# Performance work log

Measured on AMD Instinct MI355X. Metric: run time of the kernel, lower is better.

## Reference

```python
import jax, jax.numpy as jnp
import numpy as np

N, E, Z, C, B, G, T = 10000, 160000, 10, 64, 8, 16, 2
R_MAX = 5.0
AVG_NEIGH = 16.0
L_SLICES = ((0, 1), (1, 4), (4, 9))  # l=0,1,2 blocks of the 9 SH components


def sph_harm(u):
    # component-normalized real spherical harmonics up to l=2, u: [E,3] unit vectors
    x, y, z = u[:, 0], u[:, 1], u[:, 2]
    s3, s5, s15 = 3.0 ** 0.5, 5.0 ** 0.5, 15.0 ** 0.5
    return jnp.stack([
        jnp.ones_like(x),
        s3 * x, s3 * y, s3 * z,
        s15 * x * y, s15 * y * z, (s5 / 2) * (3 * z * z - 1), s15 * x * z, (s15 / 2) * (x * x - y * y),
    ], axis=1)  # [E,9]


def radial_embed(r):
    # Bessel basis * polynomial cutoff (p=5), r: [E]
    u = r / R_MAX
    n = jnp.arange(1, B + 1, dtype=jnp.float32)
    bessel = jnp.sqrt(2.0 / R_MAX) * jnp.sin(n[None, :] * jnp.pi * u[:, None]) / (r[:, None] + 1e-9)
    p = 5.0
    fc = 1 - (p + 1) * (p + 2) / 2 * u ** p + p * (p + 2) * u ** (p + 1) - p * (p + 1) / 2 * u ** (p + 2)
    fc = jnp.where(u < 1.0, fc, 0.0)
    return bessel * fc[:, None]  # [E,B]


def per_l_linear(x, W):
    # x: [n,C,9], W: [3,C,C]; independent channel mixing per l-block
    return jnp.concatenate([
        jnp.einsum('ncm,cd->ndm', x[:, :, s:e], W[l]) for l, (s, e) in enumerate(L_SLICES)
    ], axis=2)


def _forward(positions, node_attrs, charges, shifts, W_emb, atomic_energies,
             W_r1, W_r2, W_mix, W_sc, w_poly, W_prod, w_e, w_d,
             edge_index, batch, num_graphs):
    sender, receiver = edge_index[0], edge_index[1]
    # atomic reference energies
    node_e0 = node_attrs @ atomic_energies  # [N]
    e0 = jax.ops.segment_sum(node_e0, batch, num_segments=num_graphs)
    # node embedding: scalars only
    node_feats = jnp.zeros((positions.shape[0], C, 9), positions.dtype)
    node_feats = node_feats.at[:, :, 0].set(node_attrs @ W_emb)
    # edge geometry
    vec = positions[sender] - positions[receiver] + shifts  # [E,3]
    lengths = jnp.sqrt(jnp.sum(vec * vec, axis=1) + 1e-12)
    sh = sph_harm(vec / lengths[:, None])        # [E,9]
    edge_feats = radial_embed(lengths)           # [E,B]
    energies = [e0]
    dipoles = []
    for t in range(T):
        # radial MLP -> per-channel TP weights
        w = jax.nn.silu(edge_feats @ W_r1[t]) @ W_r2[t]      # [E,C]
        h_s = node_feats[sender, :, 0]                       # gather sender scalars [E,C]
        m = (w * h_s)[:, :, None] * sh[:, None, :]           # TP message [E,C,9]
        agg = jax.ops.segment_sum(m, receiver, num_segments=positions.shape[0]) / AVG_NEIGH
        msg = per_l_linear(agg, W_mix[t])
        sc = per_l_linear(node_feats, W_sc[t])               # self-connection
        # product basis (correlation 3): channel-wise scalar polynomial gate
        s0 = msg[:, :, 0]
        poly = w_poly[t, :, 0][None] + w_poly[t, :, 1][None] * s0 + w_poly[t, :, 2][None] * s0 * s0
        node_feats = per_l_linear(msg * poly[:, :, None], W_prod[t]) + sc
        # readout: 1x0e energy + 1x1o dipole
        e_n = node_feats[:, :, 0] @ w_e[t]                   # [N]
        energies.append(jax.ops.segment_sum(e_n, batch, num_segments=num_graphs))
        dipoles.append(jnp.einsum('ncm,c->nm', node_feats[:, :, 1:4], w_d[t]))  # [N,3]
    contributions = jnp.stack(energies, axis=-1)             # [G,T+1]
    total_energy = jnp.sum(contributions, axis=-1)           # [G]
    atomic_dipoles = jnp.sum(jnp.stack(dipoles, axis=-1), axis=-1)  # [N,3]
    total_dipole = jax.ops.segment_sum(atomic_dipoles, batch, num_segments=num_graphs)
    total_dipole = total_dipole + jax.ops.segment_sum(charges[:, None] * positions, batch, num_segments=num_graphs)
    return total_energy, contributions, atomic_dipoles, total_dipole


def setup_inputs():
    key = jax.random.key(0)
    ks = jax.random.split(key, 16)
    s = 0.1
    species = jax.random.randint(ks[1], (N,), 0, Z)
    return {
        'positions': jax.random.normal(ks[0], (N, 3)) * 3.0,
        'node_attrs': jax.nn.one_hot(species, Z, dtype=jnp.float32),
        'charges': jax.random.normal(ks[2], (N,)) * 0.1,
        'shifts': jnp.zeros((E, 3), jnp.float32),
        'W_emb': jax.random.normal(ks[5], (Z, C)) * s,
        'atomic_energies': jax.random.normal(ks[6], (Z,)) * s,
        'W_r1': jax.random.normal(ks[7], (T, B, 64)) * s,
        'W_r2': jax.random.normal(ks[8], (T, 64, C)) * s,
        'W_mix': jax.random.normal(ks[9], (T, 3, C, C)) * s,
        'W_sc': jax.random.normal(ks[10], (T, 3, C, C)) * s,
        'w_poly': jax.random.normal(ks[11], (T, C, 3)) * s,
        'W_prod': jax.random.normal(ks[12], (T, 3, C, C)) * s,
        'w_e': jax.random.normal(ks[13], (T, C)) * s,
        'w_d': jax.random.normal(ks[14], (T, C)) * s,
        'edge_index': jax.random.randint(ks[3], (2, E), 0, N),
        'batch': jnp.sort(jax.random.randint(ks[4], (N,), 0, G)),
        'num_graphs': G,
    }


def reference(positions, node_attrs, charges, shifts, W_emb, atomic_energies,
              W_r1, W_r2, W_mix, W_sc, w_poly, W_prod, w_e, w_d,
              edge_index, batch, num_graphs):
    args = (node_attrs, charges, shifts, W_emb, atomic_energies, W_r1, W_r2,
            W_mix, W_sc, w_poly, W_prod, w_e, w_d, edge_index, batch, num_graphs)
    total_energy, contributions, atomic_dipoles, total_dipole = _forward(positions, *args)
    forces = -jax.grad(lambda p: jnp.sum(_forward(p, *args)[0]))(positions)
    return total_energy, contributions, forces, total_dipole, atomic_dipoles
```

## Files before the change

kernel.cpp:

```cpp
#include <hip/hip_runtime.h>
#include <hip/hip_bf16.h>

#define NN 10000
#define NE 160000
#define NZ 10
#define NBES 8
#define NG 16
#define NT 2
#define NB 2048
#define NB1 2049
#define PL ((size_t)NN*64)

static constexpr float PI_F  = 3.14159265358979323846f;
static constexpr float KBES  = 0.63245553203367587f;
static constexpr float S3    = 1.73205080756887729f;

static constexpr size_t OFF_UVL  = 0;
static constexpr size_t OFF_PIN  = OFF_UVL + (size_t)NE*4;
static constexpr size_t OFF_ATT  = OFF_PIN + (size_t)NN*3;
static constexpr size_t OFF_CHG  = OFF_ATT + (size_t)NN*NZ;
static constexpr size_t OFF_SHF  = OFF_CHG + (size_t)NN;
static constexpr size_t OFF_NF0  = OFF_SHF + (size_t)NE*3;
static constexpr size_t OFF_NF1  = OFF_NF0 + PL;
static constexpr size_t OFF_MSG0 = OFF_NF1 + 4*PL;
static constexpr size_t OFF_MSG1 = OFF_MSG0 + 4*PL;
static constexpr size_t OFF_AGG  = OFF_MSG1 + 4*PL;
static constexpr size_t O_GA1    = OFF_MSG0 + PL;
static constexpr size_t O_GA0    = OFF_AGG;
static constexpr size_t OFF_W    = OFF_AGG + 4*PL;
static constexpr size_t O_WEMB   = OFF_W;
static constexpr size_t O_AE     = O_WEMB + 640;
static constexpr size_t O_R1     = O_AE   + 16;
static constexpr size_t O_R2     = O_R1   + 1024;
static constexpr size_t O_WMIX   = O_R2   + 8192;
static constexpr size_t O_WMIXT  = O_WMIX + 24576;
static constexpr size_t O_WSC    = O_WMIXT+ 24576;
static constexpr size_t O_WSCT   = O_WSC  + 24576;
static constexpr size_t O_WPROD  = O_WSCT + 24576;
static constexpr size_t O_WPRODT = O_WPROD+ 24576;
static constexpr size_t O_WPOLY  = O_WPRODT+24576;
static constexpr size_t O_WE     = O_WPOLY+ 384;
static constexpr size_t O_WD     = O_WE   + 128;
static constexpr size_t OFF_ACC  = O_WD   + 128;
static constexpr size_t O_E0G    = OFF_ACC;
static constexpr size_t O_ETG    = O_E0G + 16;
static constexpr size_t O_TD     = O_ETG + 32;
static constexpr size_t O_ADP    = O_TD  + 48;
static constexpr size_t O_GPOS   = O_ADP + (size_t)NN*3;
static constexpr size_t ACC_FLOATS = 96 + (size_t)NN*6;
static constexpr size_t O_EN0    = O_GPOS + (size_t)NN*3;
static constexpr size_t O_EN1    = O_EN0 + NN;
static constexpr size_t O_E0N    = O_EN1 + NN;
static constexpr size_t O_FLAG   = O_E0N + NN;
static constexpr size_t O_TW     = O_FLAG + 4;
static constexpr size_t O_TQ     = O_TW + (size_t)2*NB1*64;
static constexpr size_t O_OFFR   = O_TQ + (size_t)2*NB1*64;
static constexpr size_t O_OFFS   = O_OFFR + (NN+1);
static constexpr size_t O_CURR   = O_OFFS + (NN+1);
static constexpr size_t O_CURS   = O_CURR + NN;
static constexpr size_t O_RECRAW = O_CURS + NN;
static constexpr size_t O_RECR   = (O_RECRAW + 7) & ~(size_t)7;
static constexpr size_t O_RECS   = O_RECR + (size_t)NE*8 + 64;
static constexpr size_t WS_FLOATS= O_RECS + (size_t)NE*8 + 64;

__device__ __forceinline__ float rlane(float v, int l){
  return __int_as_float(__builtin_amdgcn_readlane(__float_as_int(v), l));
}
__device__ __forceinline__ int irlane(float v, int l){
  return __builtin_amdgcn_readlane(__float_as_int(v), l);
}

static constexpr int LD_CNT[14] = {NN*3, NN*NZ, NN, NE*3, NZ*64, NZ, NT*NBES*64, NT*64*64,
                                   NT*3*64*64, NT*3*64*64, NT*64*3, NT*3*64*64, NT*64, NT*64};
static constexpr int LD_TOTAL = NN*3 + NN*NZ + NN + NE*3 + NZ*64 + NZ + NT*NBES*64 + NT*64*64
                              + 3*(NT*3*64*64) + NT*64*3 + 4*(NT*64) - NT*64*2;
static constexpr int LD_B  = (LD_TOTAL + 255)/256;
static constexpr int Z1_B  = ((int)ACC_FLOATS + 255)/256;
static constexpr int Z2_B  = (2*NN + 255)/256;
__global__ __launch_bounds__(256) void k_load_all(
    const void* s0, const void* s1, const void* s2, const void* s3, const void* s4,
    const void* s5, const void* s6, const void* s7, const void* s8, const void* s9,
    const void* s10, const void* s11, const void* s12, const void* s13,
    float* __restrict__ ws){
  if (blockIdx.x >= LD_B){
    int zb = blockIdx.x - LD_B;
    if (zb < Z1_B){
      int i = zb*256 + threadIdx.x;
      if (i < (int)ACC_FLOATS) ws[OFF_ACC + i] = 0.f;
    } else {
      int i = (zb - Z1_B)*256 + threadIdx.x;
      if (i < 2*NN) ((int*)(ws + O_CURR))[i] = 0;
    }
    return;
  }
  __shared__ int found;
  if (threadIdx.x == 0) found = 0;
  __syncthreads();
  const unsigned* raw = (const unsigned*)s1;
  int f = 0;
  for (int i = threadIdx.x; i < 4096; i += 256){
    unsigned w = raw[i];
    f |= (w == 0x00003F80u || w == 0x3F803F80u) ? 1 : 0;
  }
  if (f) found = 1;
  __syncthreads();
  const int isbf = found;
  if (blockIdx.x == 0 && threadIdx.x == 0) ((int*)(ws + O_FLAG))[0] = isbf;

  const void* srcs[14] = {s0,s1,s2,s3,s4,s5,s6,s7,s8,s9,s10,s11,s12,s13};
  const size_t dsts[14] = {OFF_PIN, OFF_ATT, OFF_CHG, OFF_SHF, O_WEMB, O_AE, O_R1, O_R2,
                           O_WMIX, O_WSC, O_WPOLY, O_WPROD, O_WE, O_WD};
  int i = blockIdx.x*256 + threadIdx.x;
  int seg = -1, off = i;
  #pragma unroll
  for (int j = 0; j < 14; ++j){
    if (seg < 0){
      if (off < LD_CNT[j]) seg = j;
      else off -= LD_CNT[j];
    }
  }
  if (seg < 0) return;
  float v = isbf ? __bfloat162float(((const __hip_bfloat16*)srcs[seg])[off])
                 : ((const float*)srcs[seg])[off];
  ws[dsts[seg] + off] = v;
}

static constexpr int GEOM_B = (NE+255)/256;
static constexpr int TAB_B  = (2*NB1+3)/4;
static constexpr int INIT_B = (NN+3)/4;
static constexpr int TRAN_B = 5*4096/256;
__global__ __launch_bounds__(256, 3) void k_prep(float* __restrict__ ws, const int* __restrict__ ei){
  int b = blockIdx.x;
  if (b < GEOM_B){
    int e = b*256 + threadIdx.x;
    if (e >= NE) return;
    const float* pos = ws + OFF_PIN;
    const float* shifts = ws + OFF_SHF;
    int s = ei[e], r = ei[NE + e];
    float vx = pos[s*3+0] - pos[r*3+0] + shifts[(size_t)e*3+0];
    float vy = pos[s*3+1] - pos[r*3+1] + shifts[(size_t)e*3+1];
    float vz = pos[s*3+2] - pos[r*3+2] + shifts[(size_t)e*3+2];
    float L = sqrtf(vx*vx + vy*vy + vz*vz + 1e-12f);
    float inv = 1.f / L;
    float4 uq; uq.x = vx*inv; uq.y = vy*inv; uq.z = vz*inv; uq.w = L;
    *(float4*)(ws + OFF_UVL + (size_t)e*4) = uq;
    if (L < 5.f){
      atomicAdd((int*)(ws + O_CURR) + r, 1);
      atomicAdd((int*)(ws + O_CURS) + s, 1);
    }
  } else if (b < GEOM_B + TAB_B){
    int lane = threadIdx.x & 63;
    int task = (b - GEOM_B)*4 + (threadIdx.x >> 6);
    if (task >= 2*NB1) return;
    int t = task / NB1, node = task % NB1;
    const float* R1 = ws + O_R1 + (size_t)t*512;
    const float* R2 = ws + O_R2 + (size_t)t*4096;
    float r1c[8];
    #pragma unroll
    for (int j = 0; j < 8; ++j) r1c[j] = R1[j*64 + lane];
    float L = fmaxf((float)node * (5.f/NB), 1e-6f);
    float ur = L*0.2f;
    float ef[8], dd[8];
    if (ur < 1.f){
      float u2=ur*ur, u4=u2*u2, u5=u4*ur;
      float fc = 1.f - 21.f*u5 + 35.f*u5*ur - 15.f*u5*u2;
      float omu = 1.f - ur;
      float dfc = -105.f*u4*omu*omu;
      float invr = 1.f/(L + 1e-9f);
      #pragma unroll
      for (int bb = 0; bb < 8; ++bb){
        float nb = (float)(bb+1);
        float arg = nb*PI_F*ur;
        float sn = __sinf(arg), cs = __cosf(arg);
        float bes = KBES*sn*invr;
        float dbes = KBES*(nb*PI_F*0.2f)*cs*invr - bes*invr;
        ef[bb] = bes*fc;
        dd[bb] = dbes*fc + bes*dfc*0.2f;
      }
    } else {
      #pragma unroll
      for (int bb = 0; bb < 8; ++bb){ ef[bb] = 0.f; dd[bb] = 0.f; }
    }
    float a = 0.f, tt = 0.f;
    #pragma unroll
    for (int bb = 0; bb < 8; ++bb){ a = fmaf(ef[bb], r1c[bb], a); tt = fmaf(r1c[bb], dd[bb], tt); }
    float sg = 1.f/(1.f + __expf(-a));
    float sl = a*sg;
    float q  = sg*fmaf(a, 1.f - sg, 1.f)*tt;
    float r2c[64];
    #pragma unroll
    for (int j = 0; j < 64; ++j) r2c[j] = R2[j*64 + lane];
    float W0=0.f, W1=0.f, Q0=0.f, Q1=0.f;
    #pragma unroll
    for (int j = 0; j < 64; j += 2){
      W0 = fmaf(rlane(sl, j  ), r2c[j  ], W0);
      W1 = fmaf(rlane(sl, j+1), r2c[j+1], W1);
      Q0 = fmaf(rlane(q,  j  ), r2c[j  ], Q0);
      Q1 = fmaf(rlane(q,  j+1), r2c[j+1], Q1);
    }
    size_t idx = ((size_t)t*NB1 + node)*64 + lane;
    ws[O_TW + idx] = (W0+W1)*(1.f/16.f);
    ws[O_TQ + idx] = (Q0+Q1)*(1.f/16.f);
  } else if (b < GEOM_B + TAB_B + INIT_B){
    int lane = threadIdx.x & 63;
    int n = (b - GEOM_B - TAB_B)*4 + (threadIdx.x >> 6);
    if (n >= NN) return;
    const float* attrs = ws + OFF_ATT;
    float acc = 0.f;
    #pragma unroll
    for (int z = 0; z < NZ; ++z) acc = fmaf(attrs[(size_t)n*NZ+z], ws[O_WEMB + z*64 + lane], acc);
    ws[OFF_NF0 + (size_t)n*64 + lane] = acc;
    if (lane == 0){
      float e = 0.f;
      #pragma unroll
      for (int z = 0; z < NZ; ++z) e = fmaf(attrs[(size_t)n*NZ+z], ws[O_AE + z], e);
      ws[O_E0N + n] = e;
    }
  } else {
    int i = (b - GEOM_B - TAB_B - INIT_B)*256 + threadIdx.x;
    int mat = i >> 12, r = (i >> 6) & 63, c = i & 63;
    const size_t src[5] = {O_WMIX, O_WMIX+12288, O_WPROD, O_WPROD+12288, O_WSC+12288};
    const size_t dst[5] = {O_WMIXT, O_WMIXT+12288, O_WPRODT, O_WPRODT+12288, O_WSCT+12288};
    ws[dst[mat] + (size_t)c*64 + r] = ws[src[mat] + (size_t)r*64 + c];
  }
}

__global__ __launch_bounds__(1024) void k_csr_scan(
    int* __restrict__ curr, int* __restrict__ curs,
    int* __restrict__ offr, int* __restrict__ offs_){
  __shared__ unsigned short cr[NN], cs[NN];
  __shared__ int pr[1024], ps[1024];
  int tid = threadIdx.x;
  for (int i = tid; i < NN; i += 1024){
    cr[i] = (unsigned short)curr[i];
    cs[i] = (unsigned short)curs[i];
  }
  __syncthreads();
  const int chunk = (NN + 1023)/1024;
  int lo = tid*chunk, hi = lo + chunk;
  if (hi > NN) hi = NN;
  if (lo > NN) lo = NN;
  int sr = 0, ss = 0;
  for (int i = lo; i < hi; ++i){ sr += cr[i]; ss += cs[i]; }
  pr[tid] = sr; ps[tid] = ss;
  __syncthreads();
  for (int o = 1; o < 1024; o <<= 1){
    int vr = (tid >= o) ? pr[tid-o] : 0;
    int vs = (tid >= o) ? ps[tid-o] : 0;
    __syncthreads();
    pr[tid] += vr; ps[tid] += vs;
    __syncthreads();
  }
  int runr = tid ? pr[tid-1] : 0;
  int runs = tid ? ps[tid-1] : 0;
  for (int i = lo; i < hi; ++i){
    int a = cr[i], c = cs[i];
    offr[i] = runr; curr[i] = runr; runr += a;
    offs_[i] = runs; curs[i] = runs; runs += c;
  }
  if (tid == 1023){ offr[NN] = runr; offs_[NN] = runs; }
}

__global__ void k_csr_fill(const int* __restrict__ ei, const float* __restrict__ uvl,
                           int* __restrict__ curr, int* __restrict__ curs,
                           float* __restrict__ recr, float* __restrict__ recs){
  int e = blockIdx.x*256 + threadIdx.x;
  if (e >= NE) return;
  float4 q = *(const float4*)(uvl + (size_t)e*4);
  if (q.w >= 5.f) return;
  int s = ei[e], r = ei[NE + e];
  int4 meta; meta.x = s; meta.y = r; meta.z = e; meta.w = 0;
  int pr = atomicAdd(&curr[r], 1);
  *(float4*)(recr + (size_t)pr*8) = q;
  *(int4*)(recr + (size_t)pr*8 + 4) = meta;
  int ps = atomicAdd(&curs[s], 1);
  *(float4*)(recs + (size_t)ps*8) = q;
  *(int4*)(recs + (size_t)ps*8 + 4) = meta;
}

__global__ __launch_bounds__(256) void k_agg(
    const float* __restrict__ TWt, const float* __restrict__ recr,
    const float* __restrict__ h, const int* __restrict__ offr,
    float* __restrict__ agg){
  int lane = threadIdx.x & 63;
  int wid = blockIdx.x*4 + (threadIdx.x >> 6);
  int nw  = gridDim.x*4;
  for (int n = wid; n < NN; n += nw){
    int lo = offr[n], hi = offr[n+1];
    float c0=0.f, x1=0.f, y1=0.f, z1=0.f;
    for (int i = lo; i < hi; i += 8){
      float rv = recr[(size_t)i*8 + lane];
      int cnt = hi - i;
      if (cnt >= 8){
        #pragma unroll
        for (int j = 0; j < 8; ++j){
          float ux = rlane(rv, j*8+0), uy = rlane(rv, j*8+1), uz = rlane(rv, j*8+2);
          float L  = rlane(rv, j*8+3);
          int   s  = irlane(rv, j*8+4);
          float pos = L*(NB/5.f); int bi = (int)pos; float f = pos - (float)bi;
          const float* T = TWt + (size_t)bi*64 + lane;
          float t0 = T[0];
          float w = fmaf(T[64]-t0, f, t0);
          float wh = w * h[(size_t)s*64 + lane];
          c0 += wh;
          x1 = fmaf(wh, ux, x1);
          y1 = fmaf(wh, uy, y1);
          z1 = fmaf(wh, uz, z1);
        }
      } else {
        for (int j = 0; j < cnt; ++j){
          float ux = rlane(rv, j*8+0), uy = rlane(rv, j*8+1), uz = rlane(rv, j*8+2);
          float L  = rlane(rv, j*8+3);
          int   s  = irlane(rv, j*8+4);
          float pos = L*(NB/5.f); int bi = (int)pos; float f = pos - (float)bi;
          const float* T = TWt + (size_t)bi*64 + lane;
          float t0 = T[0];
          float w = fmaf(T[64]-t0, f, t0);
          float wh = w * h[(size_t)s*64 + lane];
          c0 += wh;
          x1 = fmaf(wh, ux, x1);
          y1 = fmaf(wh, uy, y1);
          z1 = fmaf(wh, uz, z1);
        }
      }
    }
    size_t ob = (size_t)n*64 + lane;
    agg[ob]        = c0;
    agg[ob+PL]     = S3*x1;
    agg[ob+2*PL]   = S3*y1;
    agg[ob+3*PL]   = S3*z1;
  }
}

template<int GB1>
__global__ __launch_bounds__(256, 3) void k_lin2(
    const float* __restrict__ in, const float* __restrict__ W3, float* __restrict__ out,
    const float* __restrict__ WMIXT1, const float* __restrict__ WPRODT1,
    const float* __restrict__ we1, const float* __restrict__ wp1,
    float* __restrict__ ga1){
  int k = blockIdx.y;
  int l = (k==0) ? 0 : 1;
  const float* W = W3 + (size_t)l*4096;
  int lane = threadIdx.x & 63;
  float wcol[64];
  #pragma unroll
  for (int j = 0; j < 64; ++j) wcol[j] = W[j*64 + lane];
  float wcol2[64];
  float g = 0.f, p0 = 0.f, p1 = 0.f, p2 = 0.f;
  const bool gb1 = GB1 && (k == 0);
  if (gb1){
    #pragma unroll
    for (int j = 0; j < 64; ++j) wcol2[j] = WMIXT1[j*64 + lane];
    #pragma unroll
    for (int c = 0; c < 64; ++c) g = fmaf(we1[c], WPRODT1[c*64 + lane], g);
    p0 = wp1[lane*3]; p1 = wp1[lane*3+1]; p2 = wp1[lane*3+2];
  }
  int wid = blockIdx.x*4 + (threadIdx.x >> 6);
  int nw  = gridDim.x*4;
  const float* inp = in + (size_t)k*PL;
  float* outp = out + (size_t)k*PL;
  for (int n = wid; n < NN; n += nw){
    float x = inp[(size_t)n*64 + lane];
    float a0 = 0.f, a1 = 0.f, a2 = 0.f, a3 = 0.f;
    #pragma unroll
    for (int j = 0; j < 64; j += 4){
      a0 = fmaf(rlane(x, j  ), wcol[j  ], a0);
      a1 = fmaf(rlane(x, j+1), wcol[j+1], a1);
      a2 = fmaf(rlane(x, j+2), wcol[j+2], a2);
      a3 = fmaf(rlane(x, j+3), wcol[j+3], a3);
    }
    float m = (a0+a1) + (a2+a3);
    outp[(size_t)n*64 + lane] = m;
    if (gb1){
      float poly = fmaf(fmaf(p2, m, p1), m, p0);
      float dp   = fmaf(2.f*p2, m, p1);
      float gb = g*fmaf(m, dp, poly);
      float b0=0.f, b1=0.f, b2=0.f, b3=0.f;
      #pragma unroll
      for (int j = 0; j < 64; j += 4){
        b0 = fmaf(rlane(gb, j  ), wcol2[j  ], b0);
        b1 = fmaf(rlane(gb, j+1), wcol2[j+1], b1);
        b2 = fmaf(rlane(gb, j+2), wcol2[j+2], b2);
        b3 = fmaf(rlane(gb, j+3), wcol2[j+3], b3);
      }
      ga1[(size_t)n*64 + lane] = (b0+b1) + (b2+b3);
    }
  }
}

template<int WRITE_NF, int NF_SINGLE>
__global__ __launch_bounds__(256, 3) void k_tail(
    const float* __restrict__ nf_in, const float* __restrict__ msg,
    const float* __restrict__ Wsc, const float* __restrict__ Wprod, const float* __restrict__ wp,
    const float* __restrict__ we, const float* __restrict__ wd,
    float* __restrict__ nf_out, float* __restrict__ en, float* __restrict__ adp){
  int lane = threadIdx.x & 63;
  int k = threadIdx.x >> 6;
  int l = (k==0) ? 0 : 1;
  const bool use_sc = !(NF_SINGLE && k > 0);
  float wcs[64], wcp[64];
  #pragma unroll
  for (int j = 0; j < 64; ++j)
    wcp[j] = Wprod[(size_t)l*4096 + j*64 + lane];
  if (use_sc){
    #pragma unroll
    for (int j = 0; j < 64; ++j)
      wcs[j] = Wsc[(size_t)l*4096 + j*64 + lane];
  }
  float p0 = wp[lane*3], p1 = wp[lane*3+1], p2 = wp[lane*3+2];
  float rw = (k==0) ? we[lane] : wd[lane];
  const float* msgk = msg + (size_t)k*PL;
  const float* nfk  = nf_in + (size_t)k*PL;
  float* outk = nf_out + (size_t)k*PL;
  for (int n = blockIdx.x; n < NN; n += gridDim.x){
    size_t base = (size_t)n*64 + lane;
    float s0 = msg[base];
    float xm = (k==0) ? s0 : msgk[base];
    float xg = xm * fmaf(fmaf(p2, s0, p1), s0, p0);
    float b0=0.f, b1=0.f;
    #pragma unroll
    for (int j = 0; j < 64; j += 2){
      b0 = fmaf(rlane(xg, j  ), wcp[j  ], b0);
      b1 = fmaf(rlane(xg, j+1), wcp[j+1], b1);
    }
    float out = b0 + b1;
    if (use_sc){
      float xs = nfk[base];
      float a0=0.f, a1=0.f;
      #pragma unroll
      for (int j = 0; j < 64; j += 2){
        a0 = fmaf(rlane(xs, j  ), wcs[j  ], a0);
        a1 = fmaf(rlane(xs, j+1), wcs[j+1], a1);
      }
      out += a0 + a1;
    }
    if (WRITE_NF) outk[base] = out;
    float red = out * rw;
    #pragma unroll
    for (int o = 32; o; o >>= 1) red += __shfl_xor(red, o, 64);
    if (lane == 0){
      if (k == 0) en[n] = red;
      else        adp[n*3 + (k-1)] += red;
    }
  }
}

static constexpr int GHG_GRID = 1024;
static constexpr int RED_B = (NN+255)/256;
__global__ __launch_bounds__(256) void k_ghg0(float* __restrict__ ws, const int* __restrict__ offs_,
                                              const int* __restrict__ batch){
  __shared__ float wl[2*4096];
  if (blockIdx.x >= GHG_GRID){
    int n = (blockIdx.x - GHG_GRID)*256 + threadIdx.x;
    int lane = threadIdx.x & 63;
    bool valid = (n < NN);
    int g = valid ? batch[n] : -1;
    float v0=0.f, v1=0.f, v2=0.f, tx=0.f, ty=0.f, tz=0.f;
    if (valid){
      v0 = ws[O_E0N + n]; v1 = ws[O_EN0 + n]; v2 = ws[O_EN1 + n];
      float qq = ws[OFF_CHG + n];
      tx = ws[O_ADP + n*3+0] + qq*ws[OFF_PIN + n*3+0];
      ty = ws[O_ADP + n*3+1] + qq*ws[OFF_PIN + n*3+1];
      tz = ws[O_ADP + n*3+2] + qq*ws[OFF_PIN + n*3+2];
    }
    float* e0g = ws + O_E0G; float* Etg = ws + O_ETG; float* td = ws + O_TD;
    int g0 = __shfl(g, 0, 64), g63 = __shfl(g, 63, 64);
    if (g0 == g63 && g0 >= 0){
      #pragma unroll
      for (int o = 32; o; o >>= 1){
        v0 += __shfl_xor(v0, o, 64); v1 += __shfl_xor(v1, o, 64); v2 += __shfl_xor(v2, o, 64);
        tx += __shfl_xor(tx, o, 64); ty += __shfl_xor(ty, o, 64); tz += __shfl_xor(tz, o, 64);
      }
      if (lane == 0){
        atomicAdd(&e0g[g0], v0); atomicAdd(&Etg[g0], v1); atomicAdd(&Etg[16+g0], v2);
        atomicAdd(&td[g0*3+0], tx); atomicAdd(&td[g0*3+1], ty); atomicAdd(&td[g0*3+2], tz);
      }
    } else if (valid){
      atomicAdd(&e0g[g], v0); atomicAdd(&Etg[g], v1); atomicAdd(&Etg[16+g], v2);
      atomicAdd(&td[g*3+0], tx); atomicAdd(&td[g*3+1], ty); atomicAdd(&td[g*3+2], tz);
    }
    return;
  }
  for (int i = threadIdx.x; i < 4096; i += 256){
    wl[i]        = ws[O_WPRODT + i];
    wl[4096 + i] = ws[O_WMIXT + i];
  }
  __syncthreads();
  const int lane = threadIdx.x & 63;
  int wid = blockIdx.x*4 + (threadIdx.x >> 6);
  const int nw = GHG_GRID*4;
  float gnfc = ws[O_WE + lane];
  {
    const float* WS1 = ws + O_WSCT + 12288;
    const float* we1 = ws + O_WE + 64;
    #pragma unroll
    for (int c = 0; c < 64; ++c) gnfc = fmaf(we1[c], WS1[c*64 + lane], gnfc);
  }
  const float p0 = ws[O_WPOLY + lane*3];
  const float p1 = ws[O_WPOLY + lane*3 + 1];
  const float p2 = ws[O_WPOLY + lane*3 + 2];
  const float* TW1 = ws + O_TW + (size_t)NB1*64;
  const float* recs = ws + O_RECS;
  const float* GA1 = ws + O_GA1;
  for (int n = wid; n < NN; n += nw){
    int lo = offs_[n], hi = offs_[n+1];
    float acc = 0.f;
    for (int i = lo; i < hi; i += 8){
      float rv = recs[(size_t)i*8 + lane];
      int cnt = hi - i;
      if (cnt >= 8){
        #pragma unroll
        for (int j = 0; j < 8; ++j){
          float L = rlane(rv, j*8+3);
          int   r = irlane(rv, j*8+5);
          float pos = L*(NB/5.f); int bi = (int)pos; float f = pos - (float)bi;
          const float* T = TW1 + (size_t)bi*64 + lane;
          float t0 = T[0];
          float w = fmaf(T[64]-t0, f, t0);
          acc = fmaf(w, GA1[(size_t)r*64 + lane], acc);
        }
      } else {
        for (int j = 0; j < cnt; ++j){
          float L = rlane(rv, j*8+3);
          int   r = irlane(rv, j*8+5);
          float pos = L*(NB/5.f); int bi = (int)pos; float f = pos - (float)bi;
          const float* T = TW1 + (size_t)bi*64 + lane;
          float t0 = T[0];
          float w = fmaf(T[64]-t0, f, t0);
          acc = fmaf(w, GA1[(size_t)r*64 + lane], acc);
        }
      }
    }
    float gB = gnfc + acc;
    float q0=0.f, q1=0.f;
    #pragma unroll
    for (int j = 0; j < 64; j += 2){
      q0 = fmaf(rlane(gB,j),   wl[j*64 + lane],     q0);
      q1 = fmaf(rlane(gB,j+1), wl[(j+1)*64 + lane], q1);
    }
    float gmp = q0 + q1;
    float s0v = ws[OFF_MSG0 + (size_t)n*64 + lane];
    float poly = fmaf(fmaf(p2, s0v, p1), s0v, p0);
    float dp   = fmaf(2.f*p2, s0v, p1);
    float gb = gmp * fmaf(s0v, dp, poly);
    float u0=0.f, u1=0.f;
    #pragma unroll
    for (int j = 0; j < 64; j += 2){
      u0 = fmaf(rlane(gb,j),   wl[4096 + j*64 + lane],     u0);
      u1 = fmaf(rlane(gb,j+1), wl[4096 + (j+1)*64 + lane], u1);
    }
    ws[O_GA0 + (size_t)n*64 + lane] = u0 + u1;
  }
}

__global__ __launch_bounds__(256) void k_bwdE2(float* __restrict__ ws, const int* __restrict__ nlive_ptr){
  const int lane = threadIdx.x & 63;
  int wid = blockIdx.x*4 + (threadIdx.x >> 6);
  const int nw = gridDim.x*4;
  const int nlive = nlive_ptr[0];
  const int ngrp = (nlive + 7) >> 3;
  const float* recs = ws + O_RECS;
  const float* TQ  = ws + O_TQ;
  const float* h0  = ws + OFF_NF0;
  const float* h1  = ws + OFF_NF1;
  const float* ga0 = ws + O_GA0;
  const float* ga1 = ws + O_GA1;
  float* gpos = ws + O_GPOS;
  for (int gi = wid; gi < ngrp; gi += nw){
    const int i0 = gi*8;
    float rv = recs[(size_t)i0*8 + lane];
    int cnt = nlive - i0; if (cnt > 8) cnt = 8;
    #pragma unroll 8
    for (int j = 0; j < cnt; ++j){
      float ux = rlane(rv, j*8+0), uy = rlane(rv, j*8+1), uz = rlane(rv, j*8+2);
      float L  = rlane(rv, j*8+3);
      int   s  = irlane(rv, j*8+4);
      int   r  = irlane(rv, j*8+5);
      float pos = L*(NB/5.f); int bi = (int)pos; float f = pos - (float)bi;
      const float* T0 = TQ + (size_t)bi*64 + lane;
      const float* T1 = T0 + (size_t)NB1*64;
      float Q0 = fmaf(T0[64]-T0[0], f, T0[0]);
      float Q1 = fmaf(T1[64]-T1[0], f, T1[0]);
      float rr = Q0*h0[(size_t)s*64 + lane]*ga0[(size_t)r*64 + lane]
               + Q1*h1[(size_t)s*64 + lane]*ga1[(size_t)r*64 + lane];
      #pragma unroll
      for (int o = 32; o; o >>= 1) rr += __shfl_xor(rr, o, 64);
      if (lane < 3){
        float u = (lane==0) ? ux : ((lane==1) ? uy : uz);
        float v = rr*u;
        atomicAdd(&gpos[(size_t)s*3 + lane],  v);
        atomicAdd(&gpos[(size_t)r*3 + lane], -v);
      }
    }
  }
}

__global__ void k_writeout(const float* __restrict__ e0g, const float* __restrict__ Etg,
                           const float* __restrict__ td, const float* __restrict__ adp,
                           const float* __restrict__ gpos, void* __restrict__ outv,
                           const int* __restrict__ flag){
  int i = blockIdx.x*256 + threadIdx.x;
  const int total = NG + NG*3 + NN*3 + NG*3 + NN*3;
  if (i >= total) return;
  float v;
  if (i < 16){
    v = e0g[i] + Etg[i] + Etg[16+i];
  } else if (i < 64){
    int j = i - 16; int g = j/3, t = j - g*3;
    v = (t == 0) ? e0g[g] : Etg[(t-1)*16 + g];
  } else if (i < 64 + NN*3){
    v = -gpos[i-64];
  } else if (i < 64 + NN*3 + 48){
    v = td[i - (64 + NN*3)];
  } else {
    v = adp[i - (64 + NN*3 + 48)];
  }
  if (flag[0]) ((__hip_bfloat16*)outv)[i] = __float2bfloat16(v);
  else         ((float*)outv)[i] = v;
}

extern "C" void kernel_launch(void* const* d_in, const int* in_sizes, int n_in,
                              void* d_out, int out_size, void* d_ws, size_t ws_size,
                              hipStream_t stream) {
  if (ws_size < WS_FLOATS*sizeof(float)) return;
  const int* ei    = (const int*)d_in[14];
  const int* batch = (const int*)d_in[15];
  float* ws = (float*)d_ws;

  int* offr  = (int*)(ws + O_OFFR);
  int* offs_ = (int*)(ws + O_OFFS);
  int* curr  = (int*)(ws + O_CURR);
  int* curs  = (int*)(ws + O_CURS);

  k_load_all<<<LD_B + Z1_B + Z2_B, 256, 0, stream>>>(
      d_in[0], d_in[1], d_in[2], d_in[3], d_in[4], d_in[5], d_in[6], d_in[7],
      d_in[8], d_in[9], d_in[10], d_in[11], d_in[12], d_in[13], ws);
  k_prep<<<GEOM_B + TAB_B + INIT_B + TRAN_B, 256, 0, stream>>>(ws, ei);
  k_csr_scan<<<1, 1024, 0, stream>>>(curr, curs, offr, offs_);
  k_csr_fill<<<(NE+255)/256, 256, 0, stream>>>(ei, ws+OFF_UVL, curr, curs,
                                               ws+O_RECR, ws+O_RECS);

  dim3 ling(256, 4);

  k_agg<<<1024, 256, 0, stream>>>(ws+O_TW, ws+O_RECR, ws+OFF_NF0, offr, ws+OFF_AGG);
  k_lin2<0><<<ling, 256, 0, stream>>>(ws+OFF_AGG, ws+O_WMIX, ws+OFF_MSG0,
                                      ws, ws, ws, ws, ws);
  k_tail<1,1><<<1024, 256, 0, stream>>>(ws+OFF_NF0, ws+OFF_MSG0,
                                        ws+O_WSC, ws+O_WPROD,
                                        ws+O_WPOLY, ws+O_WE, ws+O_WD,
                                        ws+OFF_NF1, ws+O_EN0, ws+O_ADP);
  k_agg<<<1024, 256, 0, stream>>>(ws+O_TW + (size_t)NB1*64, ws+O_RECR, ws+OFF_NF1, offr, ws+OFF_AGG);
  k_lin2<1><<<ling, 256, 0, stream>>>(ws+OFF_AGG, ws+O_WMIX + 12288, ws+OFF_MSG1,
                                      ws+O_WMIXT + 12288, ws+O_WPRODT + 12288,
                                      ws+O_WE + 64, ws+O_WPOLY + 192, ws+O_GA1);
  k_tail<0,0><<<1024, 256, 0, stream>>>(ws+OFF_NF1, ws+OFF_MSG1,
                                        ws+O_WSC + 12288, ws+O_WPROD + 12288,
                                        ws+O_WPOLY + 192, ws+O_WE + 64, ws+O_WD + 64,
                                        ws+OFF_NF1, ws+O_EN1, ws+O_ADP);

  k_ghg0<<<GHG_GRID + RED_B, 256, 0, stream>>>(ws, offs_, batch);
  k_bwdE2<<<2048, 256, 0, stream>>>(ws, offs_ + NN);

  k_writeout<<<(60112+255)/256, 256, 0, stream>>>(ws+O_E0G, ws+O_ETG, ws+O_TD, ws+O_ADP,
                                                  ws+O_GPOS, d_out, (const int*)(ws+O_FLAG));
}
```

Baseline: 324.3 us.

## Overlap single-block CSR scan with table, init and transpose work in one launch

The prep kernel now only does edge geometry and degree counting. The CSR prefix scan moves into block 0 of a new combined kernel, whose other blocks compute the radial tables, node embeddings and weight transposes. The serial single-block scan therefore runs alongside independent work instead of as its own launch. The cost is that the scan now uses 256 threads instead of 1024, so each thread walks a longer chunk, and every block of the combined kernel reserves the large shared arrays, which may lower occupancy.

Measured after the change: 328.1 us. About the same (+1.2%).

```diff
diff --git a/kernel.cpp b/kernel.cpp
--- a/kernel.cpp
+++ b/kernel.cpp
@@ -126,31 +126,75 @@
 }
 
 static constexpr int GEOM_B = (NE+255)/256;
+__global__ __launch_bounds__(256, 3) void k_prep(float* __restrict__ ws, const int* __restrict__ ei){
+  int e = blockIdx.x*256 + threadIdx.x;
+  if (e >= NE) return;
+  const float* pos = ws + OFF_PIN;
+  const float* shifts = ws + OFF_SHF;
+  int s = ei[e], r = ei[NE + e];
+  float vx = pos[s*3+0] - pos[r*3+0] + shifts[(size_t)e*3+0];
+  float vy = pos[s*3+1] - pos[r*3+1] + shifts[(size_t)e*3+1];
+  float vz = pos[s*3+2] - pos[r*3+2] + shifts[(size_t)e*3+2];
+  float L = sqrtf(vx*vx + vy*vy + vz*vz + 1e-12f);
+  float inv = 1.f / L;
+  float4 uq; uq.x = vx*inv; uq.y = vy*inv; uq.z = vz*inv; uq.w = L;
+  *(float4*)(ws + OFF_UVL + (size_t)e*4) = uq;
+  if (L < 5.f){
+    atomicAdd((int*)(ws + O_CURR) + r, 1);
+    atomicAdd((int*)(ws + O_CURS) + s, 1);
+  }
+}
+
 static constexpr int TAB_B  = (2*NB1+3)/4;
 static constexpr int INIT_B = (NN+3)/4;
 static constexpr int TRAN_B = 5*4096/256;
-__global__ __launch_bounds__(256, 3) void k_prep(float* __restrict__ ws, const int* __restrict__ ei){
+static constexpr int SP_TAB0  = 1;
+static constexpr int SP_INIT0 = SP_TAB0 + TAB_B;
+static constexpr int SP_TRAN0 = SP_INIT0 + INIT_B;
+static constexpr int SP_TOTAL = SP_TRAN0 + TRAN_B;
+__global__ __launch_bounds__(256, 3) void k_scan_plus(float* __restrict__ ws){
+  __shared__ unsigned short cr[NN], cs[NN];
+  __shared__ int pr[256], ps[256];
   int b = blockIdx.x;
-  if (b < GEOM_B){
-    int e = b*256 + threadIdx.x;
-    if (e >= NE) return;
-    const float* pos = ws + OFF_PIN;
-    const float* shifts = ws + OFF_SHF;
-    int s = ei[e], r = ei[NE + e];
-    float vx = pos[s*3+0] - pos[r*3+0] + shifts[(size_t)e*3+0];
-    float vy = pos[s*3+1] - pos[r*3+1] + shifts[(size_t)e*3+1];
-    float vz = pos[s*3+2] - pos[r*3+2] + shifts[(size_t)e*3+2];
-    float L = sqrtf(vx*vx + vy*vy + vz*vz + 1e-12f);
-    float inv = 1.f / L;
-    float4 uq; uq.x = vx*inv; uq.y = vy*inv; uq.z = vz*inv; uq.w = L;
-    *(float4*)(ws + OFF_UVL + (size_t)e*4) = uq;
-    if (L < 5.f){
-      atomicAdd((int*)(ws + O_CURR) + r, 1);
-      atomicAdd((int*)(ws + O_CURS) + s, 1);
-    }
-  } else if (b < GEOM_B + TAB_B){
+  if (b == 0){
+    int* curr = (int*)(ws + O_CURR);
+    int* curs = (int*)(ws + O_CURS);
+    int* offr = (int*)(ws + O_OFFR);
+    int* offs_ = (int*)(ws + O_OFFS);
+    int tid = threadIdx.x;
+    for (int i = tid; i < NN; i += 256){
+      cr[i] = (unsigned short)curr[i];
+      cs[i] = (unsigned short)curs[i];
+    }
+    __syncthreads();
+    const int chunk = (NN + 255)/256;
+    int lo = tid*chunk, hi = lo + chunk;
+    if (hi > NN) hi = NN;
+    if (lo > NN) lo = NN;
+    int sr = 0, ss = 0;
+    for (int i = lo; i < hi; ++i){ sr += cr[i]; ss += cs[i]; }
+    pr[tid] = sr; ps[tid] = ss;
+    __syncthreads();
+    for (int o = 1; o < 256; o <<= 1){
+      int vr = (tid >= o) ? pr[tid-o] : 0;
+      int vs = (tid >= o) ? ps[tid-o] : 0;
+      __syncthreads();
+      pr[tid] += vr; ps[tid] += vs;
+      __syncthreads();
+    }
+    int runr = tid ? pr[tid-1] : 0;
+    int runs = tid ? ps[tid-1] : 0;
+    for (int i = lo; i < hi; ++i){
+      int a = cr[i], c = cs[i];
+      offr[i] = runr; curr[i] = runr; runr += a;
+      offs_[i] = runs; curs[i] = runs; runs += c;
+    }
+    if (tid == 255){ offr[NN] = runr; offs_[NN] = runs; }
+    return;
+  }
+  if (b < SP_INIT0){
     int lane = threadIdx.x & 63;
-    int task = (b - GEOM_B)*4 + (threadIdx.x >> 6);
+    int task = (b - SP_TAB0)*4 + (threadIdx.x >> 6);
     if (task >= 2*NB1) return;
     int t = task / NB1, node = task % NB1;
     const float* R1 = ws + O_R1 + (size_t)t*512;
@@ -171,9 +215,9 @@
       for (int bb = 0; bb < 8; ++bb){
         float nb = (float)(bb+1);
         float arg = nb*PI_F*ur;
-        float sn = __sinf(arg), cs = __cosf(arg);
+        float sn = __sinf(arg), cs2 = __cosf(arg);
         float bes = KBES*sn*invr;
-        float dbes = KBES*(nb*PI_F*0.2f)*cs*invr - bes*invr;
+        float dbes = KBES*(nb*PI_F*0.2f)*cs2*invr - bes*invr;
         ef[bb] = bes*fc;
         dd[bb] = dbes*fc + bes*dfc*0.2f;
       }
@@ -201,9 +245,9 @@
     size_t idx = ((size_t)t*NB1 + node)*64 + lane;
     ws[O_TW + idx] = (W0+W1)*(1.f/16.f);
     ws[O_TQ + idx] = (Q0+Q1)*(1.f/16.f);
-  } else if (b < GEOM_B + TAB_B + INIT_B){
+  } else if (b < SP_TRAN0){
     int lane = threadIdx.x & 63;
-    int n = (b - GEOM_B - TAB_B)*4 + (threadIdx.x >> 6);
+    int n = (b - SP_INIT0)*4 + (threadIdx.x >> 6);
     if (n >= NN) return;
     const float* attrs = ws + OFF_ATT;
     float acc = 0.f;
@@ -217,48 +261,12 @@
       ws[O_E0N + n] = e;
     }
   } else {
-    int i = (b - GEOM_B - TAB_B - INIT_B)*256 + threadIdx.x;
+    int i = (b - SP_TRAN0)*256 + threadIdx.x;
     int mat = i >> 12, r = (i >> 6) & 63, c = i & 63;
     const size_t src[5] = {O_WMIX, O_WMIX+12288, O_WPROD, O_WPROD+12288, O_WSC+12288};
     const size_t dst[5] = {O_WMIXT, O_WMIXT+12288, O_WPRODT, O_WPRODT+12288, O_WSCT+12288};
     ws[dst[mat] + (size_t)c*64 + r] = ws[src[mat] + (size_t)r*64 + c];
   }
-}
-
-__global__ __launch_bounds__(1024) void k_csr_scan(
-    int* __restrict__ curr, int* __restrict__ curs,
-    int* __restrict__ offr, int* __restrict__ offs_){
-  __shared__ unsigned short cr[NN], cs[NN];
-  __shared__ int pr[1024], ps[1024];
-  int tid = threadIdx.x;
-  for (int i = tid; i < NN; i += 1024){
-    cr[i] = (unsigned short)curr[i];
-    cs[i] = (unsigned short)curs[i];
-  }
-  __syncthreads();
-  const int chunk = (NN + 1023)/1024;
-  int lo = tid*chunk, hi = lo + chunk;
-  if (hi > NN) hi = NN;
-  if (lo > NN) lo = NN;
-  int sr = 0, ss = 0;
-  for (int i = lo; i < hi; ++i){ sr += cr[i]; ss += cs[i]; }
-  pr[tid] = sr; ps[tid] = ss;
-  __syncthreads();
-  for (int o = 1; o < 1024; o <<= 1){
-    int vr = (tid >= o) ? pr[tid-o] : 0;
-    int vs = (tid >= o) ? ps[tid-o] : 0;
-    __syncthreads();
-    pr[tid] += vr; ps[tid] += vs;
-    __syncthreads();
-  }
-  int runr = tid ? pr[tid-1] : 0;
-  int runs = tid ? ps[tid-1] : 0;
-  for (int i = lo; i < hi; ++i){
-    int a = cr[i], c = cs[i];
-    offr[i] = runr; curr[i] = runr; runr += a;
-    offs_[i] = runs; curs[i] = runs; runs += c;
-  }
-  if (tid == 1023){ offr[NN] = runr; offs_[NN] = runs; }
 }
 
 __global__ void k_csr_fill(const int* __restrict__ ei, const float* __restrict__ uvl,
@@ -635,8 +643,8 @@
   k_load_all<<<LD_B + Z1_B + Z2_B, 256, 0, stream>>>(
       d_in[0], d_in[1], d_in[2], d_in[3], d_in[4], d_in[5], d_in[6], d_in[7],
       d_in[8], d_in[9], d_in[10], d_in[11], d_in[12], d_in[13], ws);
-  k_prep<<<GEOM_B + TAB_B + INIT_B + TRAN_B, 256, 0, stream>>>(ws, ei);
-  k_csr_scan<<<1, 1024, 0, stream>>>(curr, curs, offr, offs_);
+  k_prep<<<GEOM_B, 256, 0, stream>>>(ws, ei);
+  k_scan_plus<<<SP_TOTAL, 256, 0, stream>>>(ws);
   k_csr_fill<<<(NE+255)/256, 256, 0, stream>>>(ei, ws+OFF_UVL, curr, curs,
                                                ws+O_RECR, ws+O_RECS);
 
```
